# Kernel tuning notes

Hardware: AMD Instinct MI355X
Metric: run time of the kernel (lower is better)

The kernel has to match this reference:

```python
import jax, jax.numpy as jnp
import numpy as np

WS = (14, 14)
NUM_HEADS = 12
DIM = 768
HEAD_DIM = DIM // NUM_HEADS
N_TOK = WS[0] * WS[1] + 1  # 197 (cls token)
NUM_REL = (2 * WS[0] - 1) * (2 * WS[1] - 1) + 3  # 732
B = 64


def _build_rel_pos_index():
    ch, cw = np.arange(WS[0]), np.arange(WS[1])
    coords = np.stack(np.meshgrid(ch, cw, indexing='ij'))  # [2,h,w]
    cf = coords.reshape(2, -1)  # [2, h*w]
    rel = cf[:, :, None] - cf[:, None, :]  # [2, hw, hw]
    rel = rel.transpose(1, 2, 0).astype(np.int64)
    rel[:, :, 0] += WS[0] - 1
    rel[:, :, 1] += WS[1] - 1
    rel[:, :, 0] *= 2 * WS[1] - 1
    idx = np.zeros((N_TOK, N_TOK), dtype=np.int64)
    idx[1:, 1:] = rel.sum(-1)
    idx[0, 0:] = NUM_REL - 3
    idx[0:, 0] = NUM_REL - 2
    idx[0, 0] = NUM_REL - 1
    return idx.astype(np.int32)


def setup_inputs() -> dict:
    key = jax.random.key(0)
    ks = jax.random.split(key, 7)
    s = 0.02
    return {
        'x': jax.random.normal(ks[0], (B, N_TOK, DIM), jnp.float32),
        'qkv_w': jax.random.normal(ks[1], (3 * DIM, DIM), jnp.float32) * s,
        'q_bias': jax.random.normal(ks[2], (DIM,), jnp.float32) * s,
        'v_bias': jax.random.normal(ks[3], (DIM,), jnp.float32) * s,
        'rpb_table': jax.random.normal(ks[4], (NUM_REL, NUM_HEADS), jnp.float32) * s,
        'proj_w': jax.random.normal(ks[5], (DIM, DIM), jnp.float32) * s,
        'proj_b': jax.random.normal(ks[6], (DIM,), jnp.float32) * s,
        'rel_pos_index': jnp.asarray(_build_rel_pos_index()),
    }


def reference(x, qkv_w, q_bias, v_bias, rpb_table, proj_w, proj_b, rel_pos_index):
    Bb, N, C = x.shape
    scale = HEAD_DIM ** -0.5
    # qkv bias: [q_bias, zeros(k), v_bias]
    qkv_bias = jnp.concatenate([q_bias, jnp.zeros_like(v_bias), v_bias])
    qkv = x @ qkv_w.T + qkv_bias  # [B,N,3C]
    qkv = qkv.reshape(Bb, N, 3, NUM_HEADS, HEAD_DIM).transpose(2, 0, 3, 1, 4)
    q, k, v = qkv[0], qkv[1], qkv[2]  # [B,H,N,hd]
    attn = jnp.einsum('bhnd,bhmd->bhnm', q * scale, k)
    # gather relative position bias: [N,N,H] -> [1,H,N,N]
    rpb = rpb_table[rel_pos_index]  # [N,N,H]
    attn = attn + rpb.transpose(2, 0, 1)[None]
    attn = jax.nn.softmax(attn, axis=-1)
    out = jnp.einsum('bhnm,bhmd->bhnd', attn, v)
    out = out.transpose(0, 2, 1, 3).reshape(Bb, N, NUM_HEADS * HEAD_DIM)
    return out @ proj_w.T + proj_b
```

## Files before the change

### kernel.cpp

```cpp
#include <hip/hip_runtime.h>
#include <hip/hip_bf16.h>
#include <cstdint>
#include <cstddef>

typedef __bf16 bf16x8 __attribute__((ext_vector_type(8)));
typedef float f32x4 __attribute__((ext_vector_type(4)));

#define DI __device__ __forceinline__
#define AS1 __attribute__((address_space(1)))
#define AS3 __attribute__((address_space(3)))

DI unsigned short f2bf(float x) {
    union { float f; unsigned int u; } v; v.f = x;
    unsigned int u = v.u;
    u += 0x7FFFu + ((u >> 16) & 1u);
    return (unsigned short)(u >> 16);
}

#define BATCH 64
#define NH 12
#define NTOK 197
#define NTOK_P 208
#define HD 64
#define DIM 768
#define MROWS 12608
#define MPAD 224
#define PL4 72
#define CPAD 132
#define QSCALE 0.18033688f
#define LOG2E 1.4426950408889634f

DI int xcd_swz(int orig, int nwg) {
    int q = nwg >> 3, r = nwg & 7;
    int x = orig & 7, l = orig >> 3;
    return (x < r ? x * (q + 1) : r * (q + 1) + (x - r) * q) + l;
}

DI int swz(int row, int col_elem) {
    return (row * 64 + col_elem) ^ ((row & 7) << 3);
}


__global__ void cvt3_bf16_kernel(const float* __restrict__ a, unsigned short* __restrict__ oa, int na4,
                                 const float* __restrict__ b, unsigned short* __restrict__ ob, int nb4,
                                 const float* __restrict__ c, unsigned short* __restrict__ oc, int nc4) {
    int i = blockIdx.x * blockDim.x + threadIdx.x;
    const float* src; unsigned short* dst; int k;
    if (i < na4) { src = a; dst = oa; k = i; }
    else if (i < na4 + nb4) { src = b; dst = ob; k = i - na4; }
    else if (i < na4 + nb4 + nc4) { src = c; dst = oc; k = i - na4 - nb4; }
    else return;
    float4 f = ((const float4*)src)[k];
    ushort4 o;
    o.x = f2bf(f.x); o.y = f2bf(f.y); o.z = f2bf(f.z); o.w = f2bf(f.w);
    ((ushort4*)dst)[k] = o;
}

#define NRPB (NH * 7 * 13 * 512)
#define NPAD (BATCH * NH * HD * (MPAD - NTOK))
__global__ void prep2_kernel(const float* __restrict__ table, const int* __restrict__ idx,
                             float* __restrict__ out, unsigned short* __restrict__ vt) {
    int i = blockIdx.x * blockDim.x + threadIdx.x;
    if (i < NRPB) {
        int j = i & 3;
        int g = (i >> 2) & 1;
        int lane = (i >> 3) & 63;
        int rest = i >> 9;
        int t = rest % 13;
        int qt = (rest / 13) % 7;
        int h = rest / 91;
        int row = qt * 32 + g * 16 + ((lane >> 4) << 2) + j;
        int col = t * 16 + (lane & 15);
        float v = 0.f;
        if (row < NTOK && col < NTOK) v = table[idx[row * NTOK + col] * NH + h] * LOG2E;
        out[i] = v;
    } else if (i < NRPB + NPAD) {
        int k = i - NRPB;
        const int npad = MPAD - NTOK;
        int c = NTOK + (k % npad);
        int row = k / npad;
        vt[(size_t)row * MPAD + c] = 0;
    }
}


template<int EPI>
__launch_bounds__(256)
__global__ void gemm_bt_kernel(const unsigned short* __restrict__ A,
                               const unsigned short* __restrict__ W,
                               const float* __restrict__ bias0,
                               const float* __restrict__ bias1,
                               void* __restrict__ out0,
                               unsigned short* __restrict__ out1,
                               unsigned short* __restrict__ out2,
                               int M, int ntiles)
{
    __shared__ __align__(16) unsigned short smem[32768];
    const int K = DIM;
    const int NT = K / 64;
    int wgid = xcd_swz(blockIdx.x, gridDim.x);
    int mt = wgid / ntiles, nt = wgid % ntiles;
    int m0 = mt * 128, n0 = nt * 128;
    int tid = threadIdx.x;
    int lane = tid & 63, w = tid >> 6;
    int wr = (w >> 1) * 64, wc = (w & 1) * 64;

    const int st_row = lane >> 3;
    const int st_col = ((lane & 7) ^ (lane >> 3)) << 3;

    f32x4 acc[4][4] = {};

    auto stage = [&](int buf, int ks) {
        unsigned short* as = smem + buf * 8192;
        unsigned short* bs = smem + 16384 + buf * 8192;
#pragma unroll
        for (int i = 0; i < 4; i++) {
            int s = w * 4 + i;
            int arow = m0 + s * 8 + st_row; if (arow >= M) arow = M - 1;
            __builtin_amdgcn_global_load_lds(
                (const AS1 void*)(A + (size_t)arow * K + ks + st_col),
                (AS3 void*)(as + s * 512), 16, 0, 0);
        }
#pragma unroll
        for (int i = 0; i < 4; i++) {
            int s = w * 4 + i;
            __builtin_amdgcn_global_load_lds(
                (const AS1 void*)(W + (size_t)(n0 + s * 8 + st_row) * K + ks + st_col),
                (AS3 void*)(bs + s * 512), 16, 0, 0);
        }
    };

    stage(0, 0);
    stage(1, 64);
    asm volatile("s_waitcnt vmcnt(8)" ::: "memory");
    __builtin_amdgcn_sched_barrier(0);
    __builtin_amdgcn_s_barrier();

    for (int t = 0; t < NT; ++t) {
        int buf = t & 1;
        const unsigned short* as = smem + buf * 8192;
        const unsigned short* bs = smem + 16384 + buf * 8192;
#pragma unroll
        for (int kc = 0; kc < 2; kc++) {
            bf16x8 af[4], bfr[4];
#pragma unroll
            for (int x = 0; x < 4; x++)
                af[x] = *(const bf16x8*)&as[swz(wr + x * 16 + (lane & 15), kc * 32 + (lane >> 4) * 8)];
#pragma unroll
            for (int y = 0; y < 4; y++)
                bfr[y] = *(const bf16x8*)&bs[swz(wc + y * 16 + (lane & 15), kc * 32 + (lane >> 4) * 8)];
            __builtin_amdgcn_s_setprio(1);
#pragma unroll
            for (int x = 0; x < 4; x++)
#pragma unroll
                for (int y = 0; y < 4; y++)
                    acc[x][y] = __builtin_amdgcn_mfma_f32_16x16x32_bf16(af[x], bfr[y], acc[x][y], 0, 0, 0);
            __builtin_amdgcn_s_setprio(0);
        }
        asm volatile("s_waitcnt lgkmcnt(0)" ::: "memory");
        __builtin_amdgcn_sched_barrier(0);
        __builtin_amdgcn_s_barrier();
        if (t + 2 < NT) {
            stage(buf, (t + 2) * 64);
            asm volatile("s_waitcnt vmcnt(8)" ::: "memory");
        } else {
            asm volatile("s_waitcnt vmcnt(0)" ::: "memory");
        }
        __builtin_amdgcn_sched_barrier(0);
        __builtin_amdgcn_s_barrier();
    }

    if constexpr (EPI == 1) {
#pragma unroll
        for (int x = 0; x < 4; x++)
#pragma unroll
            for (int y = 0; y < 4; y++)
#pragma unroll
                for (int j = 0; j < 4; j++) {
                    int m = m0 + wr + x * 16 + (lane >> 4) * 4 + j;
                    int n = n0 + wc + y * 16 + (lane & 15);
                    if (m < M)
                        ((float*)out0)[(size_t)m * DIM + n] = acc[x][y][j] + bias0[n];
                }
    } else {
        int which = n0 / DIM;
        int hn0 = n0 - which * DIM;
        unsigned short* lc = smem;

        __syncthreads();
#pragma unroll
        for (int x = 0; x < 4; x++)
#pragma unroll
            for (int y = 0; y < 4; y++)
#pragma unroll
                for (int j = 0; j < 4; j++) {
                    int ml = wr + x * 16 + (lane >> 4) * 4 + j;
                    int nl = wc + y * 16 + (lane & 15);
                    float val = acc[x][y][j];
                    if (which == 0) val = (val + bias0[hn0 + nl]) * QSCALE;
                    else if (which == 2) val = val + bias1[hn0 + nl];
                    lc[ml * CPAD + nl] = f2bf(val);
                }
        __syncthreads();

        if (which != 2) {
            unsigned short* outq = (which == 0) ? (unsigned short*)out0 : out1;
            int c4 = (lane & 31) * 4;
            int h = (hn0 >> 6) + (c4 >> 6), d = c4 & 63;
            for (int it = 0; it < 16; ++it) {
                int r = it * 8 + w * 2 + (lane >> 5);
                int m = m0 + r;
                if (m >= M) continue;
                int b = m / NTOK, t = m - b * NTOK;
                ushort4 q4 = *(const ushort4*)&lc[r * CPAD + c4];
                *(ushort4*)&outq[(((size_t)b * NH + h) * NTOK_P + t) * HD + d] = q4;
            }
        } else {
            int mh = w >> 1, hs = w & 1;
            int h = (hn0 >> 6) + hs;
            int ml = mh * 64 + lane;
            int m = m0 + ml;
            if (m < M) {
                int b = m / NTOK, t = m - b * NTOK;
                unsigned short* vbase = out2 + (((size_t)b * NH + h) * HD) * MPAD + t;
#pragma unroll 8
                for (int d = 0; d < 64; ++d)
                    vbase[(size_t)d * MPAD] = lc[ml * CPAD + hs * 64 + d];
            }
        }
    }
}


__launch_bounds__(64)
__global__ void attn_kernel(const unsigned short* __restrict__ qbuf,
                            const unsigned short* __restrict__ kbuf,
                            const unsigned short* __restrict__ vt,
                            const float* __restrict__ rpb2,
                            unsigned short* __restrict__ ao)
{
    __shared__ __align__(16) unsigned short p_lds[32][PL4];
    int bid = xcd_swz(blockIdx.x, gridDim.x);
    int qt = bid % 7, bh = bid / 7;
    int b = bh / NH, h = bh - b * NH;
    int lane = threadIdx.x;
    int r0 = qt * 32;
    int col_l = lane & 15, hi = lane >> 4;

    const size_t kqbase = (size_t)bh * NTOK_P * HD;
    int qr0 = r0 + col_l;      if (qr0 > NTOK_P - 1) qr0 = NTOK_P - 1;
    int qr1 = r0 + 16 + col_l; if (qr1 > NTOK_P - 1) qr1 = NTOK_P - 1;
    bf16x8 qf0a = *(const bf16x8*)&qbuf[kqbase + (size_t)qr0 * HD + hi * 8];
    bf16x8 qf0b = *(const bf16x8*)&qbuf[kqbase + (size_t)qr0 * HD + 32 + hi * 8];
    bf16x8 qf1a = *(const bf16x8*)&qbuf[kqbase + (size_t)qr1 * HD + hi * 8];
    bf16x8 qf1b = *(const bf16x8*)&qbuf[kqbase + (size_t)qr1 * HD + 32 + hi * 8];

    const float* rpbase = rpb2 + ((size_t)(h * 7 + qt) * 13) * 512 + lane * 8;
    const size_t vbase = (size_t)bh * HD * MPAD;

    float lrow[2][4] = {};
    f32x4 o[2][4] = {};

#pragma unroll
    for (int ch = 0; ch < 4; ++ch) {
        const int t0 = ch * 4;
        const int t1 = (ch == 3) ? 13 : (t0 + 4);
#pragma unroll
        for (int t = t0; t < t1; t++) {
            int krow = t * 16 + col_l;
            bf16x8 kf0 = *(const bf16x8*)&kbuf[kqbase + (size_t)krow * HD + hi * 8];
            bf16x8 kf1 = *(const bf16x8*)&kbuf[kqbase + (size_t)krow * HD + 32 + hi * 8];
            f32x4 z = {0.f, 0.f, 0.f, 0.f};
            f32x4 sA = __builtin_amdgcn_mfma_f32_16x16x32_bf16(qf0a, kf0, z, 0, 0, 0);
            sA = __builtin_amdgcn_mfma_f32_16x16x32_bf16(qf0b, kf1, sA, 0, 0, 0);
            f32x4 sB = __builtin_amdgcn_mfma_f32_16x16x32_bf16(qf1a, kf0, z, 0, 0, 0);
            sB = __builtin_amdgcn_mfma_f32_16x16x32_bf16(qf1b, kf1, sB, 0, 0, 0);
            float4 ra = *(const float4*)&rpbase[(size_t)t * 512];
            float4 rb = *(const float4*)&rpbase[(size_t)t * 512 + 4];
            float raj[4] = {ra.x, ra.y, ra.z, ra.w};
            float rbj[4] = {rb.x, rb.y, rb.z, rb.w};
            bool masked = (t * 16 + col_l >= NTOK);
            int pc = (t - t0) * 16 + col_l;
#pragma unroll
            for (int j = 0; j < 4; j++) {
                float vA = sA[j] + raj[j];
                float vB = sB[j] + rbj[j];
                if (masked) { vA = -1e30f; vB = -1e30f; }
                float pA = exp2f(vA);
                float pB = exp2f(vB);
                lrow[0][j] += pA;
                lrow[1][j] += pB;
                p_lds[hi * 4 + j][pc] = f2bf(pA);
                p_lds[16 + hi * 4 + j][pc] = f2bf(pB);
            }
        }
        if (ch == 3) {
            ushort4 z4 = {0, 0, 0, 0};
            *(ushort4*)&p_lds[col_l][16 + hi * 4] = z4;
            *(ushort4*)&p_lds[16 + col_l][16 + hi * 4] = z4;
        }
        const int c0 = ch * 2;
        const int c1 = (ch == 3) ? 7 : (c0 + 2);
        __builtin_amdgcn_s_setprio(1);
#pragma unroll
        for (int c = c0; c < c1; c++) {
            int bcol = (c - c0) * 32;
            bf16x8 pf0 = *(const bf16x8*)&p_lds[col_l][bcol + hi * 8];
            bf16x8 pf1 = *(const bf16x8*)&p_lds[16 + col_l][bcol + hi * 8];
#pragma unroll
            for (int n = 0; n < 4; n++) {
                bf16x8 vf = *(const bf16x8*)&vt[vbase + (size_t)(n * 16 + col_l) * MPAD + c * 32 + hi * 8];
                o[0][n] = __builtin_amdgcn_mfma_f32_16x16x32_bf16(pf0, vf, o[0][n], 0, 0, 0);
                o[1][n] = __builtin_amdgcn_mfma_f32_16x16x32_bf16(pf1, vf, o[1][n], 0, 0, 0);
            }
        }
        __builtin_amdgcn_s_setprio(0);
    }

    float inv[2][4];
#pragma unroll
    for (int g = 0; g < 2; g++)
#pragma unroll
        for (int j = 0; j < 4; j++) {
            float lv = lrow[g][j];
            lv += __shfl_xor(lv, 1);
            lv += __shfl_xor(lv, 2);
            lv += __shfl_xor(lv, 4);
            lv += __shfl_xor(lv, 8);
            inv[g][j] = __builtin_amdgcn_rcpf(lv);
        }

#pragma unroll
    for (int g = 0; g < 2; g++)
#pragma unroll
        for (int n = 0; n < 4; n++)
#pragma unroll
            for (int j = 0; j < 4; j++) {
                int tok = r0 + g * 16 + hi * 4 + j;
                if (tok < NTOK) {
                    float val = o[g][n][j] * inv[g][j];
                    ao[((size_t)b * NTOK + tok) * DIM + h * HD + n * 16 + col_l] = f2bf(val);
                }
            }
}


extern "C" void kernel_launch(void* const* d_in, const int* in_sizes, int n_in,
                              void* d_out, int out_size, void* d_ws, size_t ws_size,
                              hipStream_t stream)
{
    const float* x      = (const float*)d_in[0];
    const float* qkv_w  = (const float*)d_in[1];
    const float* q_bias = (const float*)d_in[2];
    const float* v_bias = (const float*)d_in[3];
    const float* rpb_t  = (const float*)d_in[4];
    const float* proj_w = (const float*)d_in[5];
    const float* proj_b = (const float*)d_in[6];
    const int*   relidx = (const int*)d_in[7];
    float* out = (float*)d_out;

    char* ws = (char*)d_ws;
    const size_t SZ_XBF  = (size_t)MROWS * DIM * 2;
    const size_t SZ_QKVW = (size_t)3 * DIM * DIM * 2;
    const size_t SZ_PRJW = (size_t)DIM * DIM * 2;
    const size_t SZ_QK   = (size_t)BATCH * NH * NTOK_P * HD * 2;
    const size_t SZ_VT   = (size_t)BATCH * NH * HD * MPAD * 2;

    unsigned short* x_bf = (unsigned short*)ws;
    unsigned short* ao   = x_bf;
    size_t off = SZ_XBF;
    unsigned short* qkvw_bf  = (unsigned short*)(ws + off); off += SZ_QKVW;
    unsigned short* projw_bf = (unsigned short*)(ws + off); off += SZ_PRJW;
    unsigned short* qbuf     = (unsigned short*)(ws + off); off += SZ_QK;
    unsigned short* kbuf     = (unsigned short*)(ws + off); off += SZ_QK;
    unsigned short* vtbuf    = (unsigned short*)(ws + off); off += SZ_VT;
    float* rpbf              = (float*)(ws + off);

    const int NA4 = MROWS * DIM / 4, NB4 = 3 * DIM * DIM / 4, NC4 = DIM * DIM / 4;
    cvt3_bf16_kernel<<<(NA4 + NB4 + NC4 + 255) / 256, 256, 0, stream>>>(
        x, x_bf, NA4, qkv_w, qkvw_bf, NB4, proj_w, projw_bf, NC4);
    prep2_kernel<<<(NRPB + NPAD + 255) / 256, 256, 0, stream>>>(rpb_t, relidx, rpbf, vtbuf);

    gemm_bt_kernel<0><<<99 * 18, 256, 0, stream>>>(x_bf, qkvw_bf, q_bias, v_bias,
                                                   (void*)qbuf, kbuf, vtbuf, MROWS, 18);
    attn_kernel<<<BATCH * NH * 7, 64, 0, stream>>>(qbuf, kbuf, vtbuf, rpbf, ao);
    gemm_bt_kernel<1><<<99 * 6, 256, 0, stream>>>(ao, projw_bf, proj_b, nullptr,
                                                  (void*)out, nullptr, nullptr, MROWS, 6);
    (void)in_sizes; (void)n_in; (void)out_size; (void)ws_size;
}
```

Before: 168.3 us.

## Use triple-buffered K=32 stages in GEMM with packed-row LDS swizzle

The GEMM main loop moves from double-buffered K=64 tiles to triple-buffered K=32 tiles. The next stage's loads are issued before the current tile's MFMAs, and one of the two barriers per iteration is removed. A new packed LDS layout puts two rows of 32 bf16 each into a 64-element line with an XOR swizzle. LDS use drops from 64KB to 48KB, which may allow more waves per CU. The cost is twice as many iterations and a barrier on each one, each covering half as much MFMA work.

New measurement: 169.2 us. No clear change (+0.5%).

```diff
diff --git a/kernel.cpp b/kernel.cpp
--- a/kernel.cpp
+++ b/kernel.cpp
@@ -36,8 +36,10 @@
     return (x < r ? x * (q + 1) : r * (q + 1) + (x - r) * q) + l;
 }
 
-DI int swz(int row, int col_elem) {
-    return (row * 64 + col_elem) ^ ((row & 7) << 3);
+DI int pk(int r, int k) {
+    int prow = r >> 1;
+    int pcol = ((r & 1) << 5) + k;
+    return prow * 64 + (pcol ^ ((prow & 7) << 3));
 }
 
 
@@ -95,74 +97,67 @@
                                unsigned short* __restrict__ out2,
                                int M, int ntiles)
 {
-    __shared__ __align__(16) unsigned short smem[32768];
+    __shared__ __align__(16) unsigned short smem[24576];
     const int K = DIM;
-    const int NT = K / 64;
+    const int NT = 24;
     int wgid = xcd_swz(blockIdx.x, gridDim.x);
     int mt = wgid / ntiles, nt = wgid % ntiles;
     int m0 = mt * 128, n0 = nt * 128;
     int tid = threadIdx.x;
     int lane = tid & 63, w = tid >> 6;
     int wr = (w >> 1) * 64, wc = (w & 1) * 64;
-
-    const int st_row = lane >> 3;
-    const int st_col = ((lane & 7) ^ (lane >> 3)) << 3;
+    int r15 = lane & 15, hi8 = (lane >> 4) * 8;
 
     f32x4 acc[4][4] = {};
 
     auto stage = [&](int buf, int ks) {
-        unsigned short* as = smem + buf * 8192;
-        unsigned short* bs = smem + 16384 + buf * 8192;
-#pragma unroll
-        for (int i = 0; i < 4; i++) {
-            int s = w * 4 + i;
-            int arow = m0 + s * 8 + st_row; if (arow >= M) arow = M - 1;
+        unsigned short* as = smem + buf * 4096;
+        unsigned short* bs = smem + 12288 + buf * 4096;
+#pragma unroll
+        for (int r0 = 0; r0 < 2; ++r0) {
+            int L = r0 * 256 + tid;
+            int prow = L >> 3, ls = (L & 7) ^ (prow & 7);
+            int rr = (prow << 1) + (ls >> 2), kk = (ls & 3) << 3;
+            int arow = m0 + rr; if (arow >= M) arow = M - 1;
             __builtin_amdgcn_global_load_lds(
-                (const AS1 void*)(A + (size_t)arow * K + ks + st_col),
-                (AS3 void*)(as + s * 512), 16, 0, 0);
-        }
-#pragma unroll
-        for (int i = 0; i < 4; i++) {
-            int s = w * 4 + i;
+                (const AS1 void*)(A + (size_t)arow * K + ks + kk),
+                (AS3 void*)(as + r0 * 2048 + w * 512), 16, 0, 0);
             __builtin_amdgcn_global_load_lds(
-                (const AS1 void*)(W + (size_t)(n0 + s * 8 + st_row) * K + ks + st_col),
-                (AS3 void*)(bs + s * 512), 16, 0, 0);
+                (const AS1 void*)(W + (size_t)(n0 + rr) * K + ks + kk),
+                (AS3 void*)(bs + r0 * 2048 + w * 512), 16, 0, 0);
         }
     };
 
     stage(0, 0);
-    stage(1, 64);
-    asm volatile("s_waitcnt vmcnt(8)" ::: "memory");
+    stage(1, 32);
+    asm volatile("s_waitcnt vmcnt(4)" ::: "memory");
     __builtin_amdgcn_sched_barrier(0);
     __builtin_amdgcn_s_barrier();
 
     for (int t = 0; t < NT; ++t) {
-        int buf = t & 1;
-        const unsigned short* as = smem + buf * 8192;
-        const unsigned short* bs = smem + 16384 + buf * 8192;
-#pragma unroll
-        for (int kc = 0; kc < 2; kc++) {
-            bf16x8 af[4], bfr[4];
-#pragma unroll
-            for (int x = 0; x < 4; x++)
-                af[x] = *(const bf16x8*)&as[swz(wr + x * 16 + (lane & 15), kc * 32 + (lane >> 4) * 8)];
+        int cb = t % 3;
+        if (t + 2 < NT) stage((t + 2) % 3, (t + 2) * 32);
+        __builtin_amdgcn_sched_barrier(0);
+        const unsigned short* as = smem + cb * 4096;
+        const unsigned short* bs = smem + 12288 + cb * 4096;
+        bf16x8 af[4], bfr[4];
+#pragma unroll
+        for (int x = 0; x < 4; x++)
+            af[x] = *(const bf16x8*)&as[pk(wr + x * 16 + r15, hi8)];
+#pragma unroll
+        for (int y = 0; y < 4; y++)
+            bfr[y] = *(const bf16x8*)&bs[pk(wc + y * 16 + r15, hi8)];
+        __builtin_amdgcn_s_setprio(1);
+#pragma unroll
+        for (int x = 0; x < 4; x++)
 #pragma unroll
             for (int y = 0; y < 4; y++)
-                bfr[y] = *(const bf16x8*)&bs[swz(wc + y * 16 + (lane & 15), kc * 32 + (lane >> 4) * 8)];
-            __builtin_amdgcn_s_setprio(1);
-#pragma unroll
-            for (int x = 0; x < 4; x++)
-#pragma unroll
-                for (int y = 0; y < 4; y++)
-                    acc[x][y] = __builtin_amdgcn_mfma_f32_16x16x32_bf16(af[x], bfr[y], acc[x][y], 0, 0, 0);
-            __builtin_amdgcn_s_setprio(0);
-        }
+                acc[x][y] = __builtin_amdgcn_mfma_f32_16x16x32_bf16(af[x], bfr[y], acc[x][y], 0, 0, 0);
+        __builtin_amdgcn_s_setprio(0);
         asm volatile("s_waitcnt lgkmcnt(0)" ::: "memory");
         __builtin_amdgcn_sched_barrier(0);
-        __builtin_amdgcn_s_barrier();
         if (t + 2 < NT) {
-            stage(buf, (t + 2) * 64);
-            asm volatile("s_waitcnt vmcnt(8)" ::: "memory");
+            asm volatile("s_waitcnt vmcnt(4)" ::: "memory");
         } else {
             asm volatile("s_waitcnt vmcnt(0)" ::: "memory");
         }
@@ -178,7 +173,7 @@
 #pragma unroll
                 for (int j = 0; j < 4; j++) {
                     int m = m0 + wr + x * 16 + (lane >> 4) * 4 + j;
-                    int n = n0 + wc + y * 16 + (lane & 15);
+                    int n = n0 + wc + y * 16 + r15;
                     if (m < M)
                         ((float*)out0)[(size_t)m * DIM + n] = acc[x][y][j] + bias0[n];
                 }
@@ -195,7 +190,7 @@
 #pragma unroll
                 for (int j = 0; j < 4; j++) {
                     int ml = wr + x * 16 + (lane >> 4) * 4 + j;
-                    int nl = wc + y * 16 + (lane & 15);
+                    int nl = wc + y * 16 + r15;
                     float val = acc[x][y][j];
                     if (which == 0) val = (val + bias0[hn0 + nl]) * QSCALE;
                     else if (which == 2) val = val + bias1[hn0 + nl];
```

## Give output projection its own GEMM kernel with triple-buffered K=32 pipeline

Applied to the files above, without the earlier changes.

Splits the templated GEMM into a dedicated QKV kernel and a new projection kernel. The projection kernel uses 32-wide K steps with a three-stage LDS ring (48 KB instead of 64 KB) and a packed, swizzled two-rows-per-line layout. It issues the next stage's loads before the MFMAs and needs only one barrier per iteration. The aim is to raise occupancy and overlap on the small 594-block projection grid, at the cost of twice as many loop iterations and more complex address math.

After: 166.3 us. No clear change (-1.2%).

```diff
diff --git a/kernel.cpp b/kernel.cpp
--- a/kernel.cpp
+++ b/kernel.cpp
@@ -38,6 +38,12 @@
 
 DI int swz(int row, int col_elem) {
     return (row * 64 + col_elem) ^ ((row & 7) << 3);
+}
+
+DI int pk(int r, int k) {
+    int prow = r >> 1;
+    int pcol = ((r & 1) << 5) + k;
+    return prow * 64 + (pcol ^ ((prow & 7) << 3));
 }
 
 
@@ -84,16 +90,15 @@
 }
 
 
-template<int EPI>
 __launch_bounds__(256)
-__global__ void gemm_bt_kernel(const unsigned short* __restrict__ A,
-                               const unsigned short* __restrict__ W,
-                               const float* __restrict__ bias0,
-                               const float* __restrict__ bias1,
-                               void* __restrict__ out0,
-                               unsigned short* __restrict__ out1,
-                               unsigned short* __restrict__ out2,
-                               int M, int ntiles)
+__global__ void qkv_gemm_kernel(const unsigned short* __restrict__ A,
+                                const unsigned short* __restrict__ W,
+                                const float* __restrict__ bias0,
+                                const float* __restrict__ bias1,
+                                unsigned short* __restrict__ out0,
+                                unsigned short* __restrict__ out1,
+                                unsigned short* __restrict__ out2,
+                                int M, int ntiles)
 {
     __shared__ __align__(16) unsigned short smem[32768];
     const int K = DIM;
@@ -170,65 +175,139 @@
         __builtin_amdgcn_s_barrier();
     }
 
-    if constexpr (EPI == 1) {
+    int which = n0 / DIM;
+    int hn0 = n0 - which * DIM;
+    unsigned short* lc = smem;
+
+    __syncthreads();
+#pragma unroll
+    for (int x = 0; x < 4; x++)
+#pragma unroll
+        for (int y = 0; y < 4; y++)
+#pragma unroll
+            for (int j = 0; j < 4; j++) {
+                int ml = wr + x * 16 + (lane >> 4) * 4 + j;
+                int nl = wc + y * 16 + (lane & 15);
+                float val = acc[x][y][j];
+                if (which == 0) val = (val + bias0[hn0 + nl]) * QSCALE;
+                else if (which == 2) val = val + bias1[hn0 + nl];
+                lc[ml * CPAD + nl] = f2bf(val);
+            }
+    __syncthreads();
+
+    if (which != 2) {
+        unsigned short* outq = (which == 0) ? out0 : out1;
+        int c4 = (lane & 31) * 4;
+        int h = (hn0 >> 6) + (c4 >> 6), d = c4 & 63;
+        for (int it = 0; it < 16; ++it) {
+            int r = it * 8 + w * 2 + (lane >> 5);
+            int m = m0 + r;
+            if (m >= M) continue;
+            int b = m / NTOK, t = m - b * NTOK;
+            ushort4 q4 = *(const ushort4*)&lc[r * CPAD + c4];
+            *(ushort4*)&outq[(((size_t)b * NH + h) * NTOK_P + t) * HD + d] = q4;
+        }
+    } else {
+        int mh = w >> 1, hs = w & 1;
+        int h = (hn0 >> 6) + hs;
+        int ml = mh * 64 + lane;
+        int m = m0 + ml;
+        if (m < M) {
+            int b = m / NTOK, t = m - b * NTOK;
+            unsigned short* vbase = out2 + (((size_t)b * NH + h) * HD) * MPAD + t;
+#pragma unroll 8
+            for (int d = 0; d < 64; ++d)
+                vbase[(size_t)d * MPAD] = lc[ml * CPAD + hs * 64 + d];
+        }
+    }
+}
+
+
+__launch_bounds__(256)
+__global__ void proj_gemm_kernel(const unsigned short* __restrict__ A,
+                                 const unsigned short* __restrict__ W,
+                                 const float* __restrict__ bias,
+                                 float* __restrict__ out, int M, int ntiles)
+{
+    __shared__ __align__(16) unsigned short smem[24576];
+    const int K = DIM;
+    const int NT = 24;
+    int wgid = xcd_swz(blockIdx.x, gridDim.x);
+    int mt = wgid / ntiles, nt = wgid % ntiles;
+    int m0 = mt * 128, n0 = nt * 128;
+    int tid = threadIdx.x;
+    int lane = tid & 63, w = tid >> 6;
+    int wr = (w >> 1) * 64, wc = (w & 1) * 64;
+    int r15 = lane & 15, hi8 = (lane >> 4) * 8;
+
+    f32x4 acc[4][4] = {};
+
+    auto stage = [&](int buf, int ks) {
+        unsigned short* as = smem + buf * 4096;
+        unsigned short* bs = smem + 12288 + buf * 4096;
+#pragma unroll
+        for (int r0 = 0; r0 < 2; ++r0) {
+            int L = r0 * 256 + tid;
+            int prow = L >> 3, ls = (L & 7) ^ (prow & 7);
+            int rr = (prow << 1) + (ls >> 2), kk = (ls & 3) << 3;
+            int arow = m0 + rr; if (arow >= M) arow = M - 1;
+            __builtin_amdgcn_global_load_lds(
+                (const AS1 void*)(A + (size_t)arow * K + ks + kk),
+                (AS3 void*)(as + r0 * 2048 + w * 512), 16, 0, 0);
+            __builtin_amdgcn_global_load_lds(
+                (const AS1 void*)(W + (size_t)(n0 + rr) * K + ks + kk),
+                (AS3 void*)(bs + r0 * 2048 + w * 512), 16, 0, 0);
+        }
+    };
+
+    stage(0, 0);
+    stage(1, 32);
+    asm volatile("s_waitcnt vmcnt(4)" ::: "memory");
+    __builtin_amdgcn_sched_barrier(0);
+    __builtin_amdgcn_s_barrier();
+
+    for (int t = 0; t < NT; ++t) {
+        int cb = t % 3;
+        if (t + 2 < NT) stage((t + 2) % 3, (t + 2) * 32);
+        __builtin_amdgcn_sched_barrier(0);
+        const unsigned short* as = smem + cb * 4096;
+        const unsigned short* bs = smem + 12288 + cb * 4096;
+        bf16x8 af[4], bfr[4];
 #pragma unroll
         for (int x = 0; x < 4; x++)
+            af[x] = *(const bf16x8*)&as[pk(wr + x * 16 + r15, hi8)];
+#pragma unroll
+        for (int y = 0; y < 4; y++)
+            bfr[y] = *(const bf16x8*)&bs[pk(wc + y * 16 + r15, hi8)];
+        __builtin_amdgcn_s_setprio(1);
+#pragma unroll
+        for (int x = 0; x < 4; x++)
 #pragma unroll
             for (int y = 0; y < 4; y++)
-#pragma unroll
-                for (int j = 0; j < 4; j++) {
-                    int m = m0 + wr + x * 16 + (lane >> 4) * 4 + j;
-                    int n = n0 + wc + y * 16 + (lane & 15);
-                    if (m < M)
-                        ((float*)out0)[(size_t)m * DIM + n] = acc[x][y][j] + bias0[n];
-                }
-    } else {
-        int which = n0 / DIM;
-        int hn0 = n0 - which * DIM;
-        unsigned short* lc = smem;
-
-        __syncthreads();
-#pragma unroll
-        for (int x = 0; x < 4; x++)
-#pragma unroll
-            for (int y = 0; y < 4; y++)
-#pragma unroll
-                for (int j = 0; j < 4; j++) {
-                    int ml = wr + x * 16 + (lane >> 4) * 4 + j;
-                    int nl = wc + y * 16 + (lane & 15);
-                    float val = acc[x][y][j];
-                    if (which == 0) val = (val + bias0[hn0 + nl]) * QSCALE;
-                    else if (which == 2) val = val + bias1[hn0 + nl];
-                    lc[ml * CPAD + nl] = f2bf(val);
-                }
-        __syncthreads();
-
-        if (which != 2) {
-            unsigned short* outq = (which == 0) ? (unsigned short*)out0 : out1;
-            int c4 = (lane & 31) * 4;
-            int h = (hn0 >> 6) + (c4 >> 6), d = c4 & 63;
-            for (int it = 0; it < 16; ++it) {
-                int r = it * 8 + w * 2 + (lane >> 5);
-                int m = m0 + r;
-                if (m >= M) continue;
-                int b = m / NTOK, t = m - b * NTOK;
-                ushort4 q4 = *(const ushort4*)&lc[r * CPAD + c4];
-                *(ushort4*)&outq[(((size_t)b * NH + h) * NTOK_P + t) * HD + d] = q4;
+                acc[x][y] = __builtin_amdgcn_mfma_f32_16x16x32_bf16(af[x], bfr[y], acc[x][y], 0, 0, 0);
+        __builtin_amdgcn_s_setprio(0);
+        asm volatile("s_waitcnt lgkmcnt(0)" ::: "memory");
+        __builtin_amdgcn_sched_barrier(0);
+        if (t + 2 < NT) {
+            asm volatile("s_waitcnt vmcnt(4)" ::: "memory");
+        } else {
+            asm volatile("s_waitcnt vmcnt(0)" ::: "memory");
+        }
+        __builtin_amdgcn_sched_barrier(0);
+        __builtin_amdgcn_s_barrier();
+    }
+
+#pragma unroll
+    for (int x = 0; x < 4; x++)
+#pragma unroll
+        for (int y = 0; y < 4; y++)
+#pragma unroll
+            for (int j = 0; j < 4; j++) {
+                int m = m0 + wr + x * 16 + (lane >> 4) * 4 + j;
+                int n = n0 + wc + y * 16 + r15;
+                if (m < M)
+                    out[(size_t)m * DIM + n] = acc[x][y][j] + bias[n];
             }
-        } else {
-            int mh = w >> 1, hs = w & 1;
-            int h = (hn0 >> 6) + hs;
-            int ml = mh * 64 + lane;
-            int m = m0 + ml;
-            if (m < M) {
-                int b = m / NTOK, t = m - b * NTOK;
-                unsigned short* vbase = out2 + (((size_t)b * NH + h) * HD) * MPAD + t;
-#pragma unroll 8
-                for (int d = 0; d < 64; ++d)
-                    vbase[(size_t)d * MPAD] = lc[ml * CPAD + hs * 64 + d];
-            }
-        }
-    }
 }
 
 
@@ -381,10 +460,9 @@
         x, x_bf, NA4, qkv_w, qkvw_bf, NB4, proj_w, projw_bf, NC4);
     prep2_kernel<<<(NRPB + NPAD + 255) / 256, 256, 0, stream>>>(rpb_t, relidx, rpbf, vtbuf);
 
-    gemm_bt_kernel<0><<<99 * 18, 256, 0, stream>>>(x_bf, qkvw_bf, q_bias, v_bias,
-                                                   (void*)qbuf, kbuf, vtbuf, MROWS, 18);
+    qkv_gemm_kernel<<<99 * 18, 256, 0, stream>>>(x_bf, qkvw_bf, q_bias, v_bias,
+                                                 qbuf, kbuf, vtbuf, MROWS, 18);
     attn_kernel<<<BATCH * NH * 7, 64, 0, stream>>>(qbuf, kbuf, vtbuf, rpbf, ao);
-    gemm_bt_kernel<1><<<99 * 6, 256, 0, stream>>>(ao, projw_bf, proj_b, nullptr,
-                                                  (void*)out, nullptr, nullptr, MROWS, 6);
+    proj_gemm_kernel<<<99 * 6, 256, 0, stream>>>(ao, projw_bf, proj_b, out, MROWS, 6);
     (void)in_sizes; (void)n_in; (void)out_size; (void)ws_size;
 }
```
